# Optimization experiments

Hardware: AMD Instinct MI355X
Metric: run time of the kernel (lower is better)

Reference implementation:

```python
import jax, jax.numpy as jnp
import numpy as np

N_NODES = 100000
N_EDGES = 1600000
D_FEAT = 256
UNITS = 128


def setup_inputs() -> dict:
    key = jax.random.key(0)
    k1, k2, k3, k4, k5 = jax.random.split(key, 5)
    x = jax.random.normal(k1, (N_NODES, D_FEAT), dtype=jnp.float32)
    # glorot-scale init for w (scale doesn't affect correctness checking)
    w = jax.random.normal(k2, (D_FEAT, UNITS), dtype=jnp.float32) * (2.0 / (D_FEAT + UNITS)) ** 0.5
    adj_src = jax.random.randint(k3, (N_EDGES,), 0, N_NODES, dtype=jnp.int64)
    adj_dst = jax.random.randint(k4, (N_EDGES,), 0, N_NODES, dtype=jnp.int64)
    adj_vals = jax.random.uniform(k5, (N_EDGES,), dtype=jnp.float32)
    return {"x": x, "w": w, "adj_src": adj_src, "adj_dst": adj_dst, "adj_vals": adj_vals}


def reference(x, w, adj_src, adj_dst, adj_vals):
    # x: [N, D], w: [D, U]  -> dense projection
    h = x @ w  # [N, U]
    # sparse_dense_matmul(adj_norm, h): out[i] = sum_j A[i,j] * h[j]
    # COO: edge e contributes adj_vals[e] * h[adj_src[e]] to row adj_dst[e]
    msgs = adj_vals[:, None] * h[adj_src]  # [E, U]
    out = jax.ops.segment_sum(msgs, adj_dst, num_segments=N_NODES)  # [N, U]
    return out
```

## Files before the change

kernel.cpp:

```cpp
#include <hip/hip_runtime.h>

#define D_FEAT 256
#define UNITS  128

#define NBITS  6
#define BINSZ  64
#define BINCAP 1280
#define MAXNB  1600

typedef __attribute__((ext_vector_type(8))) short short8;
typedef __attribute__((ext_vector_type(4))) float floatx4;

__device__ inline ushort f2bf(float f) {
    uint u = __float_as_uint(f);
    uint r = u + 0x7FFF + ((u >> 16) & 1);
    return (ushort)(r >> 16);
}

__global__ __launch_bounds__(256) void wt_prep_kernel(const float* __restrict__ w,
                                                      ushort* __restrict__ wT) {
    int idx = blockIdx.x * 256 + threadIdx.x;
    int n = idx >> 8;
    int k = idx & 255;
    wT[n * 256 + k] = f2bf(w[(size_t)k * UNITS + n]);
}

__global__ __launch_bounds__(256, 2) void gemm_mfma3_kernel(const float* __restrict__ x,
                                                            const ushort* __restrict__ wT,
                                                            ushort* __restrict__ hb, int M) {
    __shared__ ushort lds_w[128 * 256];

    const int tid  = threadIdx.x;
    const int wave = tid >> 6;
    const int lane = tid & 63;
    const int quad = lane >> 4;
    const int m16  = lane & 15;

    const int row  = blockIdx.x * 64 + wave * 16 + m16;
    const int rowc = row < M ? row : M - 1;
    const float* xr = x + (size_t)rowc * D_FEAT;

    short8 wv[16];
    #pragma unroll
    for (int r = 0; r < 16; ++r)
        wv[r] = *(const short8*)(wT + (size_t)(r * 256 + tid) * 8);
    __builtin_amdgcn_sched_barrier(0);

    float4 xv[16];
    #pragma unroll
    for (int s = 0; s < 8; ++s) {
        const float4* p = (const float4*)(xr + s * 32 + quad * 8);
        xv[2 * s]     = p[0];
        xv[2 * s + 1] = p[1];
    }
    __builtin_amdgcn_sched_barrier(0);

    #pragma unroll
    for (int r = 0; r < 16; ++r) {
        int ci = r * 256 + tid;
        int n  = ci >> 5;
        int ts = (ci & 31) ^ (n & 7);
        *(short8*)(lds_w + n * 256 + ts * 8) = wv[r];
    }
    __builtin_amdgcn_sched_barrier(0);

    short8 afrag[8];
    #pragma unroll
    for (int s = 0; s < 8; ++s) {
        float4 lo = xv[2 * s];
        float4 hi = xv[2 * s + 1];
        union { short8 v; ushort u[8]; } af;
        af.u[0] = f2bf(lo.x); af.u[1] = f2bf(lo.y);
        af.u[2] = f2bf(lo.z); af.u[3] = f2bf(lo.w);
        af.u[4] = f2bf(hi.x); af.u[5] = f2bf(hi.y);
        af.u[6] = f2bf(hi.z); af.u[7] = f2bf(hi.w);
        afrag[s] = af.v;
    }

    __syncthreads();

    floatx4 acc[8] = {};
    #pragma unroll
    for (int s = 0; s < 8; ++s) {
        #pragma unroll
        for (int c = 0; c < 8; ++c) {
            int rowb = c * 16 + m16;
            int ts   = (s * 4 + quad) ^ (m16 & 7);
            short8 bfrag = *(const short8*)(lds_w + rowb * 256 + ts * 8);
            acc[c] = __builtin_amdgcn_mfma_f32_16x16x32_bf16(afrag[s], bfrag, acc[c], 0, 0, 0);
        }
    }

    #pragma unroll
    for (int c = 0; c < 8; ++c) {
        #pragma unroll
        for (int i = 0; i < 4; ++i) {
            int r = blockIdx.x * 64 + wave * 16 + quad * 4 + i;
            if (r < M) hb[(size_t)r * UNITS + c * 16 + m16] = f2bf(acc[c][i]);
        }
    }
}

__global__ __launch_bounds__(1024) void coarse_scatter_kernel(const int* __restrict__ src,
                                                              const int* __restrict__ dst,
                                                              const float* __restrict__ vals,
                                                              int* __restrict__ cursor,
                                                              int2* __restrict__ staged,
                                                              int E, int NB, int chunk) {
    __shared__ int s_hist[MAXNB];
    __shared__ int s_base[MAXNB];

    const int tid = threadIdx.x;
    const int T   = 1024;
    const int e0 = blockIdx.x * chunk;
    const int e1 = min(E, e0 + chunk);

    for (int i = tid; i < NB; i += T) s_hist[i] = 0;
    __syncthreads();

    for (int e = e0 + tid; e < e1; e += T)
        atomicAdd(&s_hist[dst[e] >> NBITS], 1);
    __syncthreads();

    for (int b = tid; b < NB; b += T) {
        int c = s_hist[b];
        s_base[b] = (c > 0) ? atomicAdd(&cursor[b * 4], c) : 0;
    }
    __syncthreads();
    for (int i = tid; i < NB; i += T) s_hist[i] = 0;
    __syncthreads();

    for (int e = e0 + tid; e < e1; e += T) {
        int d = dst[e];
        int b = d >> NBITS;
        int r = s_base[b] + atomicAdd(&s_hist[b], 1);
        if (r < BINCAP) {
            int meta = src[e] | ((d & (BINSZ - 1)) << 20);
            staged[(size_t)b * BINCAP + r] = make_int2(meta, __float_as_int(vals[e]));
        }
    }
}

__global__ __launch_bounds__(512) void gather_sort_kernel(const int* __restrict__ cursor,
                                                          const int2* __restrict__ staged,
                                                          const ushort* __restrict__ hb,
                                                          float* __restrict__ out, int N) {
    __shared__ int2 sraw[BINCAP];
    __shared__ int2 sbuf[BINCAP];
    __shared__ int cnt[BINSZ], ofs[BINSZ], cur[BINSZ];
    __shared__ int gofs[8];

    const int b   = blockIdx.x;
    const int tid = threadIdx.x;

    int n = cursor[b * 4];
    if (n > BINCAP) n = BINCAP;

    for (int i = tid; i < BINSZ; i += 512) cnt[i] = 0;
    __syncthreads();

    const int2* sg = staged + (size_t)b * BINCAP;

    for (int i = tid; i < n; i += 512) {
        int2 e = sg[i];
        sraw[i] = e;
        atomicAdd(&cnt[(e.x >> 20) & (BINSZ - 1)], 1);
    }
    __syncthreads();

    if (tid < 8) {
        int s = 0;
        #pragma unroll
        for (int j = 0; j < 8; ++j) s += cnt[tid * 8 + j];
        gofs[tid] = s;
    }
    __syncthreads();
    if (tid == 0) {
        int run = 0;
        #pragma unroll
        for (int g = 0; g < 8; ++g) { int c = gofs[g]; gofs[g] = run; run += c; }
    }
    __syncthreads();
    if (tid < 8) {
        int run = gofs[tid];
        #pragma unroll
        for (int j = 0; j < 8; ++j) {
            int d = tid * 8 + j;
            int c = cnt[d];
            ofs[d] = run; cur[d] = run; run += c;
        }
    }
    __syncthreads();

    for (int i = tid; i < n; i += 512) {
        int2 e = sraw[i];
        int pos = atomicAdd(&cur[(e.x >> 20) & (BINSZ - 1)], 1);
        sbuf[pos] = e;
    }
    __syncthreads();

    const int half = tid >> 5;
    const int lane = tid & 31;

    for (int d0 = 0; d0 < BINSZ; d0 += 16) {
        int d  = d0 + half;
        int dg = b * BINSZ + d;
        if (dg >= N) continue;
        int start = ofs[d];
        int c     = cnt[d];

        float a0 = 0.f, a1 = 0.f, a2 = 0.f, a3 = 0.f;
        float b0 = 0.f, b1 = 0.f, b2 = 0.f, b3 = 0.f;
        float c0 = 0.f, c1 = 0.f, c2 = 0.f, c3 = 0.f;
        float d0_ = 0.f, d1_ = 0.f, d2_ = 0.f, d3_ = 0.f;
        int j = 0;
        for (; j + 4 <= c; j += 4) {
            int2 ea = sbuf[start + j];
            int2 eb = sbuf[start + j + 1];
            int2 ec = sbuf[start + j + 2];
            int2 ed = sbuf[start + j + 3];
            uint2 ha = *(const uint2*)(hb + (size_t)(ea.x & 0xFFFFF) * UNITS + lane * 4);
            uint2 hc = *(const uint2*)(hb + (size_t)(eb.x & 0xFFFFF) * UNITS + lane * 4);
            uint2 he = *(const uint2*)(hb + (size_t)(ec.x & 0xFFFFF) * UNITS + lane * 4);
            uint2 hg = *(const uint2*)(hb + (size_t)(ed.x & 0xFFFFF) * UNITS + lane * 4);
            float va = __int_as_float(ea.y);
            float vb = __int_as_float(eb.y);
            float vc = __int_as_float(ec.y);
            float vd = __int_as_float(ed.y);
            a0 += va * __uint_as_float(ha.x << 16);
            a1 += va * __uint_as_float(ha.x & 0xFFFF0000u);
            a2 += va * __uint_as_float(ha.y << 16);
            a3 += va * __uint_as_float(ha.y & 0xFFFF0000u);
            b0 += vb * __uint_as_float(hc.x << 16);
            b1 += vb * __uint_as_float(hc.x & 0xFFFF0000u);
            b2 += vb * __uint_as_float(hc.y << 16);
            b3 += vb * __uint_as_float(hc.y & 0xFFFF0000u);
            c0 += vc * __uint_as_float(he.x << 16);
            c1 += vc * __uint_as_float(he.x & 0xFFFF0000u);
            c2 += vc * __uint_as_float(he.y << 16);
            c3 += vc * __uint_as_float(he.y & 0xFFFF0000u);
            d0_ += vd * __uint_as_float(hg.x << 16);
            d1_ += vd * __uint_as_float(hg.x & 0xFFFF0000u);
            d2_ += vd * __uint_as_float(hg.y << 16);
            d3_ += vd * __uint_as_float(hg.y & 0xFFFF0000u);
        }
        for (; j < c; ++j) {
            int2 ea = sbuf[start + j];
            uint2 ha = *(const uint2*)(hb + (size_t)(ea.x & 0xFFFFF) * UNITS + lane * 4);
            float va = __int_as_float(ea.y);
            a0 += va * __uint_as_float(ha.x << 16);
            a1 += va * __uint_as_float(ha.x & 0xFFFF0000u);
            a2 += va * __uint_as_float(ha.y << 16);
            a3 += va * __uint_as_float(ha.y & 0xFFFF0000u);
        }
        float4 r = make_float4(a0 + b0 + c0 + d0_,
                               a1 + b1 + c1 + d1_,
                               a2 + b2 + c2 + d2_,
                               a3 + b3 + c3 + d3_);
        *(float4*)(out + (size_t)dg * UNITS + lane * 4) = r;
    }
}

extern "C" void kernel_launch(void* const* d_in, const int* in_sizes, int n_in,
                              void* d_out, int out_size, void* d_ws, size_t ws_size,
                              hipStream_t stream) {
    const float* x        = (const float*)d_in[0];
    const float* w        = (const float*)d_in[1];
    const int*   adj_src  = (const int*)d_in[2];
    const int*   adj_dst  = (const int*)d_in[3];
    const float* adj_vals = (const float*)d_in[4];
    float*       out      = (float*)d_out;

    const int M = in_sizes[0] / D_FEAT;
    const int E = in_sizes[2];
    const int NB = (M + BINSZ - 1) >> NBITS;

    char*   ws  = (char*)d_ws;
    ushort* hb  = (ushort*)ws;
    size_t  off = (size_t)M * UNITS * sizeof(ushort);
    off = (off + 255) & ~(size_t)255;
    ushort* wT  = (ushort*)(ws + off);
    off += (size_t)128 * 256 * sizeof(ushort);
    int*    cursor = (int*)(ws + off);
    off += (size_t)NB * 4 * sizeof(int);
    off = (off + 15) & ~(size_t)15;
    int2*   staged = (int2*)(ws + off);

    hipMemsetAsync(cursor, 0, (size_t)NB * 4 * sizeof(int), stream);

    wt_prep_kernel<<<128, 256, 0, stream>>>(w, wT);

    gemm_mfma3_kernel<<<(M + 63) / 64, 256, 0, stream>>>(x, wT, hb, M);

    const int NSCAT = 256;
    const int chunk = (E + NSCAT - 1) / NSCAT;
    coarse_scatter_kernel<<<NSCAT, 1024, 0, stream>>>(adj_src, adj_dst, adj_vals,
                                                      cursor, staged, E, NB, chunk);

    gather_sort_kernel<<<NB, 512, 0, stream>>>(cursor, staged, hb, out, M);
}
```

Before: 287.1 us.

## Locally sort edges by bin in LDS before scatter; widen gather loads

The coarse scatter kernel now uses a fixed edge chunk per block and counting-sorts the chunk's edges by destination bin in shared memory, using a hierarchical prefix scan. It then writes them out contiguously per bin, so global stores to the staged buffer are grouped rather than scattered. The gather phase changes to 16 lanes per destination row with 16-byte loads and 8 accumulators, and writes its output with nontemporal stores. The cost is much larger shared-memory use in the scatter kernel, which lowers occupancy, and the gather loses the four independent partial-sum chains it had before.

```diff
diff --git a/kernel.cpp b/kernel.cpp
--- a/kernel.cpp
+++ b/kernel.cpp
@@ -7,6 +7,7 @@
 #define BINSZ  64
 #define BINCAP 1280
 #define MAXNB  1600
+#define SCHUNK 6400
 
 typedef __attribute__((ext_vector_type(8))) short short8;
 typedef __attribute__((ext_vector_type(4))) float floatx4;
@@ -106,40 +107,99 @@
                                                               const float* __restrict__ vals,
                                                               int* __restrict__ cursor,
                                                               int2* __restrict__ staged,
-                                                              int E, int NB, int chunk) {
-    __shared__ int s_hist[MAXNB];
-    __shared__ int s_base[MAXNB];
+                                                              int E, int NB) {
+    __shared__ int    s_cnt[MAXNB];
+    __shared__ int    s_start[MAXNB];
+    __shared__ int    s_base[MAXNB];
+    __shared__ int    s_g[256];
+    __shared__ int    s_h[32];
+    __shared__ int2   s_sort[SCHUNK];
+    __shared__ ushort s_bin[SCHUNK];
 
     const int tid = threadIdx.x;
-    const int T   = 1024;
-    const int e0 = blockIdx.x * chunk;
-    const int e1 = min(E, e0 + chunk);
-
-    for (int i = tid; i < NB; i += T) s_hist[i] = 0;
-    __syncthreads();
-
-    for (int e = e0 + tid; e < e1; e += T)
-        atomicAdd(&s_hist[dst[e] >> NBITS], 1);
-    __syncthreads();
-
-    for (int b = tid; b < NB; b += T) {
-        int c = s_hist[b];
-        s_base[b] = (c > 0) ? atomicAdd(&cursor[b * 4], c) : 0;
-    }
-    __syncthreads();
-    for (int i = tid; i < NB; i += T) s_hist[i] = 0;
-    __syncthreads();
-
-    for (int e = e0 + tid; e < e1; e += T) {
-        int d = dst[e];
-        int b = d >> NBITS;
-        int r = s_base[b] + atomicAdd(&s_hist[b], 1);
-        if (r < BINCAP) {
-            int meta = src[e] | ((d & (BINSZ - 1)) << 20);
-            staged[(size_t)b * BINCAP + r] = make_int2(meta, __float_as_int(vals[e]));
-        }
-    }
-}
+    const int e0  = blockIdx.x * SCHUNK;
+    const int e1  = min(E, e0 + SCHUNK);
+    const int tot = e1 - e0;
+
+    for (int i = tid; i < NB; i += 1024) s_cnt[i] = 0;
+    __syncthreads();
+
+    for (int e = e0 + tid; e < e1; e += 1024)
+        atomicAdd(&s_cnt[dst[e] >> NBITS], 1);
+    __syncthreads();
+
+    const int NG = (NB + 7) >> 3;
+    const int NH = (NG + 7) >> 3;
+    if (tid < NG) {
+        int s = 0;
+        #pragma unroll
+        for (int j = 0; j < 8; ++j) { int bb = tid * 8 + j; if (bb < NB) s += s_cnt[bb]; }
+        s_g[tid] = s;
+    }
+    __syncthreads();
+    if (tid < NH) {
+        int s = 0;
+        #pragma unroll
+        for (int j = 0; j < 8; ++j) { int gg = tid * 8 + j; if (gg < NG) s += s_g[gg]; }
+        s_h[tid] = s;
+    }
+    __syncthreads();
+    if (tid == 0) {
+        int run = 0;
+        for (int k = 0; k < NH; ++k) { int c = s_h[k]; s_h[k] = run; run += c; }
+    }
+    __syncthreads();
+    if (tid < NH) {
+        int run = s_h[tid];
+        #pragma unroll
+        for (int j = 0; j < 8; ++j) {
+            int gg = tid * 8 + j;
+            if (gg < NG) { int c = s_g[gg]; s_g[gg] = run; run += c; }
+        }
+    }
+    __syncthreads();
+    if (tid < NG) {
+        int run = s_g[tid];
+        #pragma unroll
+        for (int j = 0; j < 8; ++j) {
+            int bb = tid * 8 + j;
+            if (bb < NB) {
+                int c = s_cnt[bb];
+                s_start[bb] = run; run += c;
+                s_base[bb]  = (c > 0) ? atomicAdd(&cursor[bb * 4], c) : 0;
+            }
+        }
+    }
+    __syncthreads();
+    for (int i = tid; i < NB; i += 1024) s_cnt[i] = s_start[i];
+    __syncthreads();
+
+    for (int e = e0 + tid; e < e1; e += 1024) {
+        int d  = dst[e];
+        int bb = d >> NBITS;
+        int r  = atomicAdd(&s_cnt[bb], 1);
+        s_sort[r] = make_int2(src[e] | ((d & (BINSZ - 1)) << 20), __float_as_int(vals[e]));
+        s_bin[r]  = (ushort)bb;
+    }
+    __syncthreads();
+
+    for (int i = tid; i < tot; i += 1024) {
+        int bb   = s_bin[i];
+        int gpos = s_base[bb] + (i - s_start[bb]);
+        if (gpos < BINCAP)
+            staged[(size_t)bb * BINCAP + gpos] = s_sort[i];
+    }
+}
+
+#define ACC8(h, v)                                  \
+    a0 += (v) * __uint_as_float((h).x << 16);       \
+    a1 += (v) * __uint_as_float((h).x & 0xFFFF0000u); \
+    a2 += (v) * __uint_as_float((h).y << 16);       \
+    a3 += (v) * __uint_as_float((h).y & 0xFFFF0000u); \
+    a4 += (v) * __uint_as_float((h).z << 16);       \
+    a5 += (v) * __uint_as_float((h).z & 0xFFFF0000u); \
+    a6 += (v) * __uint_as_float((h).w << 16);       \
+    a7 += (v) * __uint_as_float((h).w & 0xFFFF0000u);
 
 __global__ __launch_bounds__(512) void gather_sort_kernel(const int* __restrict__ cursor,
                                                           const int2* __restrict__ staged,
@@ -199,65 +259,50 @@
     }
     __syncthreads();
 
-    const int half = tid >> 5;
-    const int lane = tid & 31;
-
-    for (int d0 = 0; d0 < BINSZ; d0 += 16) {
-        int d  = d0 + half;
+    const int ex = (tid >> 6) * 4 + ((tid & 63) >> 4);
+    const int m  = tid & 15;
+
+    #pragma unroll
+    for (int r = 0; r < 2; ++r) {
+        int d  = r * 32 + ex;
         int dg = b * BINSZ + d;
         if (dg >= N) continue;
         int start = ofs[d];
         int c     = cnt[d];
 
         float a0 = 0.f, a1 = 0.f, a2 = 0.f, a3 = 0.f;
-        float b0 = 0.f, b1 = 0.f, b2 = 0.f, b3 = 0.f;
-        float c0 = 0.f, c1 = 0.f, c2 = 0.f, c3 = 0.f;
-        float d0_ = 0.f, d1_ = 0.f, d2_ = 0.f, d3_ = 0.f;
+        float a4 = 0.f, a5 = 0.f, a6 = 0.f, a7 = 0.f;
         int j = 0;
         for (; j + 4 <= c; j += 4) {
-            int2 ea = sbuf[start + j];
-            int2 eb = sbuf[start + j + 1];
-            int2 ec = sbuf[start + j + 2];
-            int2 ed = sbuf[start + j + 3];
-            uint2 ha = *(const uint2*)(hb + (size_t)(ea.x & 0xFFFFF) * UNITS + lane * 4);
-            uint2 hc = *(const uint2*)(hb + (size_t)(eb.x & 0xFFFFF) * UNITS + lane * 4);
-            uint2 he = *(const uint2*)(hb + (size_t)(ec.x & 0xFFFFF) * UNITS + lane * 4);
-            uint2 hg = *(const uint2*)(hb + (size_t)(ed.x & 0xFFFFF) * UNITS + lane * 4);
-            float va = __int_as_float(ea.y);
-            float vb = __int_as_float(eb.y);
-            float vc = __int_as_float(ec.y);
-            float vd = __int_as_float(ed.y);
-            a0 += va * __uint_as_float(ha.x << 16);
-            a1 += va * __uint_as_float(ha.x & 0xFFFF0000u);
-            a2 += va * __uint_as_float(ha.y << 16);
-            a3 += va * __uint_as_float(ha.y & 0xFFFF0000u);
-            b0 += vb * __uint_as_float(hc.x << 16);
-            b1 += vb * __uint_as_float(hc.x & 0xFFFF0000u);
-            b2 += vb * __uint_as_float(hc.y << 16);
-            b3 += vb * __uint_as_float(hc.y & 0xFFFF0000u);
-            c0 += vc * __uint_as_float(he.x << 16);
-            c1 += vc * __uint_as_float(he.x & 0xFFFF0000u);
-            c2 += vc * __uint_as_float(he.y << 16);
-            c3 += vc * __uint_as_float(he.y & 0xFFFF0000u);
-            d0_ += vd * __uint_as_float(hg.x << 16);
-            d1_ += vd * __uint_as_float(hg.x & 0xFFFF0000u);
-            d2_ += vd * __uint_as_float(hg.y << 16);
-            d3_ += vd * __uint_as_float(hg.y & 0xFFFF0000u);
+            int2 e0 = sbuf[start + j];
+            int2 e1 = sbuf[start + j + 1];
+            int2 e2 = sbuf[start + j + 2];
+            int2 e3 = sbuf[start + j + 3];
+            uint4 h0 = *(const uint4*)(hb + (size_t)(e0.x & 0xFFFFF) * UNITS + m * 8);
+            uint4 h1 = *(const uint4*)(hb + (size_t)(e1.x & 0xFFFFF) * UNITS + m * 8);
+            uint4 h2 = *(const uint4*)(hb + (size_t)(e2.x & 0xFFFFF) * UNITS + m * 8);
+            uint4 h3 = *(const uint4*)(hb + (size_t)(e3.x & 0xFFFFF) * UNITS + m * 8);
+            float v0 = __int_as_float(e0.y);
+            float v1 = __int_as_float(e1.y);
+            float v2 = __int_as_float(e2.y);
+            float v3 = __int_as_float(e3.y);
+            ACC8(h0, v0)
+            ACC8(h1, v1)
+            ACC8(h2, v2)
+            ACC8(h3, v3)
         }
         for (; j < c; ++j) {
-            int2 ea = sbuf[start + j];
-            uint2 ha = *(const uint2*)(hb + (size_t)(ea.x & 0xFFFFF) * UNITS + lane * 4);
-            float va = __int_as_float(ea.y);
-            a0 += va * __uint_as_float(ha.x << 16);
-            a1 += va * __uint_as_float(ha.x & 0xFFFF0000u);
-            a2 += va * __uint_as_float(ha.y << 16);
-            a3 += va * __uint_as_float(ha.y & 0xFFFF0000u);
-        }
-        float4 r = make_float4(a0 + b0 + c0 + d0_,
-                               a1 + b1 + c1 + d1_,
-                               a2 + b2 + c2 + d2_,
-                               a3 + b3 + c3 + d3_);
-        *(float4*)(out + (size_t)dg * UNITS + lane * 4) = r;
+            int2 e0 = sbuf[start + j];
+            uint4 h0 = *(const uint4*)(hb + (size_t)(e0.x & 0xFFFFF) * UNITS + m * 8);
+            float v0 = __int_as_float(e0.y);
+            ACC8(h0, v0)
+        }
+
+        float* op = out + (size_t)dg * UNITS + m * 8;
+        floatx4 r0 = {a0, a1, a2, a3};
+        floatx4 r1 = {a4, a5, a6, a7};
+        __builtin_nontemporal_store(r0, (floatx4*)op);
+        __builtin_nontemporal_store(r1, (floatx4*)(op + 4));
     }
 }
 
@@ -292,10 +337,9 @@
 
     gemm_mfma3_kernel<<<(M + 63) / 64, 256, 0, stream>>>(x, wT, hb, M);
 
-    const int NSCAT = 256;
-    const int chunk = (E + NSCAT - 1) / NSCAT;
+    const int NSCAT = (E + SCHUNK - 1) / SCHUNK;
     coarse_scatter_kernel<<<NSCAT, 1024, 0, stream>>>(adj_src, adj_dst, adj_vals,
-                                                      cursor, staged, E, NB, chunk);
+                                                      cursor, staged, E, NB);
 
     gather_sort_kernel<<<NB, 512, 0, stream>>>(cursor, staged, hb, out, M);
 }
```

Measured after the change: 297.4 us. 3.6% more time.
